# Performance work log

Hardware: AMD Instinct MI355X
Metric: run time of the kernel (lower is better)

Reference implementation:

```python
import jax, jax.numpy as jnp
import numpy as np

N_NODES = 100000
N_EDGES = 1600000
IN_DIM = 64
OUT_DIM = 64
HIDDEN = 64  # fixed in edge_weight_mlp
POS_DIM = 3


def setup_inputs() -> dict:
    key = jax.random.key(0)
    ks = jax.random.split(key, 10)
    x = jax.random.normal(ks[0], (N_NODES, IN_DIM), dtype=jnp.float32)
    edge_index = jax.random.randint(ks[1], (2, N_EDGES), 0, N_NODES, dtype=jnp.int64)
    pos = jax.random.normal(ks[2], (N_NODES, POS_DIM), dtype=jnp.float32)
    # edge_weight_mlp params: Linear(2*IN_DIM+1 -> 64), Linear(64 -> 1)
    s1 = 1.0 / np.sqrt(2 * IN_DIM + 1)
    w1 = jax.random.uniform(ks[3], (2 * IN_DIM + 1, HIDDEN), jnp.float32, -s1, s1)
    b1 = jax.random.uniform(ks[4], (HIDDEN,), jnp.float32, -s1, s1)
    s2 = 1.0 / np.sqrt(HIDDEN)
    w2 = jax.random.uniform(ks[5], (HIDDEN, 1), jnp.float32, -s2, s2)
    b2 = jax.random.uniform(ks[6], (1,), jnp.float32, -s2, s2)
    # transform: Linear(IN_DIM -> OUT_DIM)
    st = 1.0 / np.sqrt(IN_DIM)
    wt = jax.random.uniform(ks[7], (IN_DIM, OUT_DIM), jnp.float32, -st, st)
    bt = jax.random.uniform(ks[8], (OUT_DIM,), jnp.float32, -st, st)
    return {"x": x, "edge_index": edge_index, "pos": pos,
            "w1": w1, "b1": b1, "w2": w2, "b2": b2, "wt": wt, "bt": bt}


def reference(x, edge_index, pos, w1, b1, w2, b2, wt, bt):
    src, dst = edge_index[0], edge_index[1]
    # edge weights: MLP on [x_src, x_dst, |pos_dst - pos_src|]
    edge_length = jnp.linalg.norm(pos[dst] - pos[src], axis=1, keepdims=True)  # [E,1]
    edge_feat = jnp.concatenate([x[src], x[dst], edge_length], axis=1)  # [E, 2*in+1]
    h = jax.nn.relu(edge_feat @ w1 + b1)
    edge_weights = jax.nn.sigmoid(h @ w2 + b2)  # [E,1]
    # node transform, gather, weight, scatter-add
    x_t = x @ wt + bt  # [N, out]
    messages = x_t[src] * edge_weights  # [E, out]
    out = jax.ops.segment_sum(messages, dst, num_segments=x.shape[0])  # [N, out]
    return out, edge_weights
```

## Files before the change

kernel.cpp:

```cpp
#include <hip/hip_runtime.h>
#include <hip/hip_bf16.h>
#include <math.h>

#define NN 100000
#define NE 1600000
#define CAP 48
#define NB 391
#define BCAP 4608
#define EPB 4096
#define NBLKA ((NE + EPB - 1) / EPB)
#define NPREP ((NN + 63) / 64)
#define PSTR 72

typedef __attribute__((ext_vector_type(8))) short short8;
typedef __attribute__((ext_vector_type(4))) float floatx4;
typedef __attribute__((ext_vector_type(2))) float float2v;

#if __has_builtin(__builtin_elementwise_fma)
#define VFMA(a, b, c) __builtin_elementwise_fma((a), (b), (c))
#else
#define VFMA(a, b, c) ((a) * (b) + (c))
#endif

static __device__ __forceinline__ unsigned short f2bb(float f) {
    __hip_bfloat16 h = __float2bfloat16(f);
    return *(unsigned short*)&h;
}
static __device__ __forceinline__ float hi_f(unsigned u) {
    return __uint_as_float(u & 0xFFFF0000u);
}
static __device__ __forceinline__ float lo_f(unsigned u) {
    return __uint_as_float(u << 16);
}
static __device__ __forceinline__ float2v hi2(unsigned a, unsigned b) {
    float2v r; r.x = __uint_as_float(a & 0xFFFF0000u);
    r.y = __uint_as_float(b & 0xFFFF0000u); return r;
}
static __device__ __forceinline__ float2v lo2(unsigned a, unsigned b) {
    float2v r; r.x = __uint_as_float(a << 16);
    r.y = __uint_as_float(b << 16); return r;
}

__global__ __launch_bounds__(256) void fused_prep_bucket(
    const float* __restrict__ x, const float* __restrict__ w1,
    const float* __restrict__ b1, const float* __restrict__ pos,
    const int* __restrict__ ei,
    unsigned int* __restrict__ rec, unsigned short* __restrict__ hd,
    float4* __restrict__ pos4, int* __restrict__ gcursor,
    uint2* __restrict__ bucketed) {
    __shared__ __align__(16) unsigned char smem[(64 + 128) * PSTR * 2];
    int t = threadIdx.x;
    if (blockIdx.x < NPREP) {
        unsigned short* As = (unsigned short*)smem;
        unsigned short* Bs = As + 64 * PSTR;
        int nbase = blockIdx.x * 64;
        {
            int r = t & 63;
            int node = nbase + r; if (node >= NN) node = NN - 1;
            const float4* xr = (const float4*)(x + (size_t)node * 64);
#pragma unroll
            for (int i = 0; i < 4; ++i) {
                int s = (t >> 6) + 4 * i;
                float4 v = xr[s];
                ushort4 o = {f2bb(v.x), f2bb(v.y), f2bb(v.z), f2bb(v.w)};
                *(ushort4*)&As[r * PSTR + s * 4] = o;
            }
        }
        {
            int n = t & 127;
            int kh = t >> 7;
            int krow = (n < 64) ? 0 : 64;
            int col = n & 63;
#pragma unroll
            for (int i = 0; i < 32; ++i) {
                int k = kh * 32 + i;
                Bs[n * PSTR + k] = f2bb(w1[(krow + k) * 64 + col]);
            }
        }
        if (t < 64) {
            int node = nbase + t;
            if (node < NN)
                pos4[node] = make_float4(pos[node * 3 + 0], pos[node * 3 + 1],
                                         pos[node * 3 + 2], 0.f);
        }
        __syncthreads();
        int lane = t & 63, wave = t >> 6;
        int grp = lane >> 4, l15 = lane & 15;
        floatx4 acc[8] = {};
        int arow = wave * 16 + l15;
#pragma unroll
        for (int ks = 0; ks < 2; ++ks) {
            int koff = ks * 32 + grp * 8;
            short8 a = *(const short8*)&As[arow * PSTR + koff];
#pragma unroll
            for (int nt = 0; nt < 8; ++nt) {
                short8 b = *(const short8*)&Bs[(nt * 16 + l15) * PSTR + koff];
                acc[nt] = __builtin_amdgcn_mfma_f32_16x16x32_bf16(a, b, acc[nt], 0, 0, 0);
            }
        }
#pragma unroll
        for (int nt = 0; nt < 8; ++nt) {
#pragma unroll
            for (int r = 0; r < 4; ++r) {
                int nr = wave * 16 + grp * 4 + r;
                int node = nbase + nr;
                if (node >= NN) continue;
                if (nt < 4) {
                    int col = nt * 16 + l15;
                    unsigned xbits = As[nr * PSTR + col];
                    rec[(size_t)node * 64 + col] =
                        ((unsigned)f2bb(acc[nt][r]) << 16) | xbits;
                } else {
                    int col = (nt - 4) * 16 + l15;
                    hd[(size_t)node * 64 + col] = f2bb(acc[nt][r] + b1[col]);
                }
            }
        }
    } else {
        int* cnt = (int*)smem;
        int* base_s = cnt + NB;
        for (int i = t; i < NB; i += 256) cnt[i] = 0;
        __syncthreads();
        int e0 = (blockIdx.x - NPREP) * EPB;
        unsigned int tags[16];
        int srcs[16], dsts[16];
#pragma unroll
        for (int i = 0; i < 16; ++i) {
            int e = e0 + i * 256 + t;
            tags[i] = 0xFFFFFFFFu;
            if (e < NE) {
                srcs[i] = ei[e];
                dsts[i] = ei[NE + e];
                int b = dsts[i] >> 8;
                int slot = atomicAdd(&cnt[b], 1);
                tags[i] = ((unsigned)b << 12) | (unsigned)slot;
            }
        }
        __syncthreads();
        for (int b = t; b < NB; b += 256)
            base_s[b] = atomicAdd(&gcursor[b], cnt[b]);
        __syncthreads();
#pragma unroll
        for (int i = 0; i < 16; ++i) {
            if (tags[i] != 0xFFFFFFFFu) {
                int e = e0 + i * 256 + t;
                int b = (int)(tags[i] >> 12);
                int slot = (int)(tags[i] & 0xFFFu);
                int p = base_s[b] + slot;
                if (p < BCAP) {
                    bucketed[(size_t)b * BCAP + p] =
                        make_uint2((unsigned)srcs[i] |
                                   (((unsigned)dsts[i] & 255u) << 17),
                                   (unsigned)e);
                }
            }
        }
    }
}

__global__ __launch_bounds__(1024) void csr_kernel(
    const uint2* __restrict__ bucketed, const int* __restrict__ gcursor,
    uint2* __restrict__ pairs, int* __restrict__ deg) {
    __shared__ int cur[256];
    int t = threadIdx.x;
    if (t < 256) cur[t] = 0;
    __syncthreads();
    int b = blockIdx.x;
    int n0 = b << 8;
    int cnt = gcursor[b];
    if (cnt > BCAP) cnt = BCAP;
    for (int i = t; i < cnt; i += 1024) {
        uint2 en = bucketed[(size_t)b * BCAP + i];
        int dwb = (int)((en.x >> 17) & 255u);
        unsigned src = en.x & 0x1FFFFu;
        int slot = atomicAdd(&cur[dwb], 1);
        if (slot < CAP)
            pairs[(size_t)(n0 + dwb) * CAP + slot] = make_uint2(src, en.y);
    }
    __syncthreads();
    if (t < 256) {
        int node = n0 + t;
        if (node < NN) deg[node] = (cur[t] > CAP) ? CAP : cur[t];
    }
}

__global__ __launch_bounds__(256) void mega_kernel(
    const uint2* __restrict__ pairs, const int* __restrict__ deg,
    const unsigned int* __restrict__ rec, const unsigned short* __restrict__ hd,
    const float4* __restrict__ pos4, const float* __restrict__ w1,
    const float* __restrict__ w2, const float* __restrict__ b2,
    float* __restrict__ ew_out, unsigned short* __restrict__ aggb,
    float* __restrict__ sumw) {
    int t = threadIdx.x;
    int w = t >> 6, lane = t & 63;
    int e8 = lane >> 3, hg = lane & 7;
    int node = blockIdx.x * 4 + w;
    if (node >= NN) return;

    const float2v zero2 = {0.f, 0.f};
    float2v a01 = zero2, a23 = zero2, a45 = zero2, a67 = zero2;
    float sw = 0.f;
    int d = deg[node];
    uint4 hz = ((const uint4*)(hd + (size_t)node * 64))[hg];
    float2v zb01 = {lo_f(hz.x), hi_f(hz.x)};
    float2v zb23 = {lo_f(hz.y), hi_f(hz.y)};
    float2v zb45 = {lo_f(hz.z), hi_f(hz.z)};
    float2v zb67 = {lo_f(hz.w), hi_f(hz.w)};
    const float2v* w2p = (const float2v*)(w2 + 8 * hg);
    float2v w20 = w2p[0], w21 = w2p[1], w22 = w2p[2], w23 = w2p[3];
    const float2v* wlp = (const float2v*)(w1 + 128 * 64 + 8 * hg);
    float2v wl0 = wlp[0], wl1 = wlp[1], wl2 = wlp[2], wl3 = wlp[3];
    float4 pd = pos4[node];
    float b2v = b2[0];
    const uint2* seg = pairs + (size_t)node * CAP;
    const uint4* rec4 = (const uint4*)rec;

    if (d > 0) {
        int i0 = (e8 < d) ? e8 : (d - 1);
        uint2 pr_c = seg[i0];
        uint2 pr_n = pr_c;
        if (8 < d) { int i1 = (8 + e8 < d) ? (8 + e8) : (d - 1); pr_n = seg[i1]; }
        uint4 ua_c = rec4[(size_t)pr_c.x * 16 + 2 * hg];
        uint4 ub_c = rec4[(size_t)pr_c.x * 16 + 2 * hg + 1];
        float4 ps_c = pos4[pr_c.x];

#pragma unroll 2
        for (int j = 0; j < d; j += 8) {
            int jn = j + 8;
            uint2 pr_n2 = pr_n;
            uint4 ua_n = ua_c, ub_n = ub_c;
            float4 ps_n = ps_c;
            if (jn < d) {
                ua_n = rec4[(size_t)pr_n.x * 16 + 2 * hg];
                ub_n = rec4[(size_t)pr_n.x * 16 + 2 * hg + 1];
                ps_n = pos4[pr_n.x];
                if (jn + 8 < d) {
                    int i2 = (jn + 8 + e8 < d) ? (jn + 8 + e8) : (d - 1);
                    pr_n2 = seg[i2];
                }
            }
            bool valid = (j + e8 < d);
            float dx = pd.x - ps_c.x;
            float dy = pd.y - ps_c.y;
            float dz = pd.z - ps_c.z;
            float len = __builtin_amdgcn_sqrtf(dx * dx + dy * dy + dz * dz);
            float2v l2; l2.x = len; l2.y = len;
            float2v z, r, tp;
            z = zb01 + hi2(ua_c.x, ua_c.y); z = VFMA(l2, wl0, z);
            r = __builtin_elementwise_max(z, zero2); tp = r * w20;
            z = zb23 + hi2(ua_c.z, ua_c.w); z = VFMA(l2, wl1, z);
            r = __builtin_elementwise_max(z, zero2); tp = VFMA(r, w21, tp);
            z = zb45 + hi2(ub_c.x, ub_c.y); z = VFMA(l2, wl2, z);
            r = __builtin_elementwise_max(z, zero2); tp = VFMA(r, w22, tp);
            z = zb67 + hi2(ub_c.z, ub_c.w); z = VFMA(l2, wl3, z);
            r = __builtin_elementwise_max(z, zero2); tp = VFMA(r, w23, tp);
            float tt = tp.x + tp.y;
            tt += __shfl_xor(tt, 1);
            tt += __shfl_xor(tt, 2);
            tt += __shfl_xor(tt, 4);
            float ew = __builtin_amdgcn_rcpf(1.f + __expf(-(tt + b2v)));
            if (valid) {
                if (hg == 0) ew_out[pr_c.y] = ew;
                float2v e2; e2.x = ew; e2.y = ew;
                a01 = VFMA(e2, lo2(ua_c.x, ua_c.y), a01);
                a23 = VFMA(e2, lo2(ua_c.z, ua_c.w), a23);
                a45 = VFMA(e2, lo2(ub_c.x, ub_c.y), a45);
                a67 = VFMA(e2, lo2(ub_c.z, ub_c.w), a67);
                sw += ew;
            }
            pr_c = pr_n; pr_n = pr_n2;
            ua_c = ua_n; ub_c = ub_n; ps_c = ps_n;
        }
    }
    float acc0 = a01.x, acc1 = a01.y, acc2 = a23.x, acc3 = a23.y;
    float acc4 = a45.x, acc5 = a45.y, acc6 = a67.x, acc7 = a67.y;
#pragma unroll
    for (int off = 8; off < 64; off <<= 1) {
        acc0 += __shfl_xor(acc0, off);
        acc1 += __shfl_xor(acc1, off);
        acc2 += __shfl_xor(acc2, off);
        acc3 += __shfl_xor(acc3, off);
        acc4 += __shfl_xor(acc4, off);
        acc5 += __shfl_xor(acc5, off);
        acc6 += __shfl_xor(acc6, off);
        acc7 += __shfl_xor(acc7, off);
        sw   += __shfl_xor(sw, off);
    }
    if (e8 == 0) {
        uint4 o;
        o.x = ((unsigned)f2bb(acc1) << 16) | f2bb(acc0);
        o.y = ((unsigned)f2bb(acc3) << 16) | f2bb(acc2);
        o.z = ((unsigned)f2bb(acc5) << 16) | f2bb(acc4);
        o.w = ((unsigned)f2bb(acc7) << 16) | f2bb(acc6);
        *(uint4*)(aggb + (size_t)node * 64 + hg * 8) = o;
    }
    if (lane == 0) sumw[node] = sw;
}

__global__ __launch_bounds__(256) void transform_mfma(
    const unsigned short* __restrict__ aggb, const float* __restrict__ sumw,
    const float* __restrict__ wt, const float* __restrict__ bt,
    float* __restrict__ out) {
    __shared__ unsigned short As[64 * PSTR];
    __shared__ unsigned short Bs[64 * PSTR];
    int t = threadIdx.x;
    int nbase = blockIdx.x * 64;
    {
        int r = t & 63;
        int node = nbase + r; if (node >= NN) node = NN - 1;
        const uint4* ar = (const uint4*)(aggb + (size_t)node * 64);
#pragma unroll
        for (int i = 0; i < 2; ++i) {
            int s = (t >> 6) + 4 * i;
            *(uint4*)&As[r * PSTR + s * 8] = ar[s];
        }
    }
    {
        int n = t & 63;
        int kq = t >> 6;
#pragma unroll
        for (int i = 0; i < 16; ++i) {
            int k = kq * 16 + i;
            Bs[n * PSTR + k] = f2bb(wt[k * 64 + n]);
        }
    }
    __syncthreads();
    int lane = t & 63, wave = t >> 6;
    int grp = lane >> 4, l15 = lane & 15;
    floatx4 acc[4] = {};
    int arow = wave * 16 + l15;
#pragma unroll
    for (int ks = 0; ks < 2; ++ks) {
        int koff = ks * 32 + grp * 8;
        short8 a = *(const short8*)&As[arow * PSTR + koff];
#pragma unroll
        for (int nt = 0; nt < 4; ++nt) {
            short8 b = *(const short8*)&Bs[(nt * 16 + l15) * PSTR + koff];
            acc[nt] = __builtin_amdgcn_mfma_f32_16x16x32_bf16(a, b, acc[nt], 0, 0, 0);
        }
    }
#pragma unroll
    for (int nt = 0; nt < 4; ++nt) {
        int col = nt * 16 + l15;
        float btv = bt[col];
#pragma unroll
        for (int r = 0; r < 4; ++r) {
            int node = nbase + wave * 16 + grp * 4 + r;
            if (node < NN)
                out[(size_t)node * 64 + col] = acc[nt][r] + sumw[node] * btv;
        }
    }
}

extern "C" void kernel_launch(void* const* d_in, const int* in_sizes, int n_in,
                              void* d_out, int out_size, void* d_ws, size_t ws_size,
                              hipStream_t stream) {
    const float* x   = (const float*)d_in[0];
    const int*   ei  = (const int*)d_in[1];
    const float* pos = (const float*)d_in[2];
    const float* w1  = (const float*)d_in[3];
    const float* b1  = (const float*)d_in[4];
    const float* w2  = (const float*)d_in[5];
    const float* b2  = (const float*)d_in[6];
    const float* wt  = (const float*)d_in[7];
    const float* bt  = (const float*)d_in[8];

    float* out    = (float*)d_out;
    float* ew_out = out + (size_t)NN * 64;

    unsigned int* rec = (unsigned int*)d_ws;
    unsigned short* hd = (unsigned short*)(rec + (size_t)NN * 64);
    uint2* pairs = (uint2*)(hd + (size_t)NN * 64);
    unsigned short* aggb = (unsigned short*)(pairs + (size_t)NN * CAP);
    float4* pos4 = (float4*)(aggb + (size_t)NN * 64);
    float* sumw = (float*)(pos4 + NN);
    int* gcursor = (int*)(sumw + NN);
    int* deg = gcursor + NB;

    uint2* bucketed = (uint2*)d_out;

    hipMemsetAsync(gcursor, 0, NB * sizeof(int), stream);
    fused_prep_bucket<<<NPREP + NBLKA, 256, 0, stream>>>(
        x, w1, b1, pos, ei, rec, hd, pos4, gcursor, bucketed);
    csr_kernel<<<NB, 1024, 0, stream>>>(bucketed, gcursor, pairs, deg);
    mega_kernel<<<(NN + 3) / 4, 256, 0, stream>>>(pairs, deg, rec, hd, pos4,
                                                  w1, w2, b2, ew_out, aggb, sumw);
    transform_mfma<<<(NN + 63) / 64, 256, 0, stream>>>(aggb, sumw, wt, bt, out);
}
```

Before: 246.0 us.

## Build per-node CSR directly with global atomics, dropping bucket pass and csr kernel

Replaces the two-stage bucketing (shared-memory bucket counts, global cursor, then a separate csr_kernel) with direct global atomicAdd on a per-node degree counter that writes each edge into its node's fixed-capacity slot. This removes one kernel launch and the intermediate bucketed buffer round-trip through memory. The cost is 1.6M global atomics scattered over 100K counters and scattered 8-byte writes into pairs, which may contend or give poorer write locality. Degree is now clamped to CAP in mega_kernel, and a larger memset clears the degree array.

Result: slower. 316.4 us (+28.6%).

```diff
diff --git a/kernel.cpp b/kernel.cpp
--- a/kernel.cpp
+++ b/kernel.cpp
@@ -5,8 +5,6 @@
 #define NN 100000
 #define NE 1600000
 #define CAP 48
-#define NB 391
-#define BCAP 4608
 #define EPB 4096
 #define NBLKA ((NE + EPB - 1) / EPB)
 #define NPREP ((NN + 63) / 64)
@@ -46,8 +44,8 @@
     const float* __restrict__ b1, const float* __restrict__ pos,
     const int* __restrict__ ei,
     unsigned int* __restrict__ rec, unsigned short* __restrict__ hd,
-    float4* __restrict__ pos4, int* __restrict__ gcursor,
-    uint2* __restrict__ bucketed) {
+    float4* __restrict__ pos4, int* __restrict__ deg,
+    uint2* __restrict__ pairs) {
     __shared__ __align__(16) unsigned char smem[(64 + 128) * PSTR * 2];
     int t = threadIdx.x;
     if (blockIdx.x < NPREP) {
@@ -117,70 +115,19 @@
             }
         }
     } else {
-        int* cnt = (int*)smem;
-        int* base_s = cnt + NB;
-        for (int i = t; i < NB; i += 256) cnt[i] = 0;
-        __syncthreads();
         int e0 = (blockIdx.x - NPREP) * EPB;
-        unsigned int tags[16];
-        int srcs[16], dsts[16];
-#pragma unroll
+#pragma unroll 4
         for (int i = 0; i < 16; ++i) {
             int e = e0 + i * 256 + t;
-            tags[i] = 0xFFFFFFFFu;
             if (e < NE) {
-                srcs[i] = ei[e];
-                dsts[i] = ei[NE + e];
-                int b = dsts[i] >> 8;
-                int slot = atomicAdd(&cnt[b], 1);
-                tags[i] = ((unsigned)b << 12) | (unsigned)slot;
-            }
-        }
-        __syncthreads();
-        for (int b = t; b < NB; b += 256)
-            base_s[b] = atomicAdd(&gcursor[b], cnt[b]);
-        __syncthreads();
-#pragma unroll
-        for (int i = 0; i < 16; ++i) {
-            if (tags[i] != 0xFFFFFFFFu) {
-                int e = e0 + i * 256 + t;
-                int b = (int)(tags[i] >> 12);
-                int slot = (int)(tags[i] & 0xFFFu);
-                int p = base_s[b] + slot;
-                if (p < BCAP) {
-                    bucketed[(size_t)b * BCAP + p] =
-                        make_uint2((unsigned)srcs[i] |
-                                   (((unsigned)dsts[i] & 255u) << 17),
-                                   (unsigned)e);
-                }
-            }
-        }
-    }
-}
-
-__global__ __launch_bounds__(1024) void csr_kernel(
-    const uint2* __restrict__ bucketed, const int* __restrict__ gcursor,
-    uint2* __restrict__ pairs, int* __restrict__ deg) {
-    __shared__ int cur[256];
-    int t = threadIdx.x;
-    if (t < 256) cur[t] = 0;
-    __syncthreads();
-    int b = blockIdx.x;
-    int n0 = b << 8;
-    int cnt = gcursor[b];
-    if (cnt > BCAP) cnt = BCAP;
-    for (int i = t; i < cnt; i += 1024) {
-        uint2 en = bucketed[(size_t)b * BCAP + i];
-        int dwb = (int)((en.x >> 17) & 255u);
-        unsigned src = en.x & 0x1FFFFu;
-        int slot = atomicAdd(&cur[dwb], 1);
-        if (slot < CAP)
-            pairs[(size_t)(n0 + dwb) * CAP + slot] = make_uint2(src, en.y);
-    }
-    __syncthreads();
-    if (t < 256) {
-        int node = n0 + t;
-        if (node < NN) deg[node] = (cur[t] > CAP) ? CAP : cur[t];
+                int src = ei[e];
+                int dst = ei[NE + e];
+                int slot = atomicAdd(&deg[dst], 1);
+                if (slot < CAP)
+                    pairs[(size_t)dst * CAP + slot] =
+                        make_uint2((unsigned)src, (unsigned)e);
+            }
+        }
     }
 }
 
@@ -201,6 +148,7 @@
     float2v a01 = zero2, a23 = zero2, a45 = zero2, a67 = zero2;
     float sw = 0.f;
     int d = deg[node];
+    if (d > CAP) d = CAP;
     uint4 hz = ((const uint4*)(hd + (size_t)node * 64))[hg];
     float2v zb01 = {lo_f(hz.x), hi_f(hz.x)};
     float2v zb23 = {lo_f(hz.y), hi_f(hz.y)};
@@ -374,15 +322,11 @@
     unsigned short* aggb = (unsigned short*)(pairs + (size_t)NN * CAP);
     float4* pos4 = (float4*)(aggb + (size_t)NN * 64);
     float* sumw = (float*)(pos4 + NN);
-    int* gcursor = (int*)(sumw + NN);
-    int* deg = gcursor + NB;
-
-    uint2* bucketed = (uint2*)d_out;
-
-    hipMemsetAsync(gcursor, 0, NB * sizeof(int), stream);
+    int* deg = (int*)(sumw + NN);
+
+    hipMemsetAsync(deg, 0, NN * sizeof(int), stream);
     fused_prep_bucket<<<NPREP + NBLKA, 256, 0, stream>>>(
-        x, w1, b1, pos, ei, rec, hd, pos4, gcursor, bucketed);
-    csr_kernel<<<NB, 1024, 0, stream>>>(bucketed, gcursor, pairs, deg);
+        x, w1, b1, pos, ei, rec, hd, pos4, deg, pairs);
     mega_kernel<<<(NN + 3) / 4, 256, 0, stream>>>(pairs, deg, rec, hd, pos4,
                                                   w1, w2, b2, ew_out, aggb, sumw);
     transform_mfma<<<(NN + 63) / 64, 256, 0, stream>>>(aggb, sumw, wt, bt, out);
```

## Apply node transform before aggregation and drop separate transform kernel

Applied to the files above, without the earlier changes.

The prep kernel now also multiplies x by wt with MFMA and stores bf16 x@wt in the low half of each rec word, where it previously stored bf16 x. The edge-aggregation kernel then sums already-transformed features, adds sumw*bt, and writes the fp32 output directly. This rests on linearity, since a weighted sum of x rows times wt equals the weighted sum of the transformed rows. It removes the transform_mfma launch and the write and re-read of the aggb and sumw intermediates. The cost is extra MFMA work and weight staging in the prep kernel, plus bf16 rounding now applied to x@wt instead of to x.

After: 238.8 us. 1.03x faster.

```diff
diff --git a/kernel.cpp b/kernel.cpp
--- a/kernel.cpp
+++ b/kernel.cpp
@@ -43,12 +43,12 @@
 
 __global__ __launch_bounds__(256) void fused_prep_bucket(
     const float* __restrict__ x, const float* __restrict__ w1,
-    const float* __restrict__ b1, const float* __restrict__ pos,
-    const int* __restrict__ ei,
+    const float* __restrict__ b1, const float* __restrict__ wt,
+    const float* __restrict__ pos, const int* __restrict__ ei,
     unsigned int* __restrict__ rec, unsigned short* __restrict__ hd,
     float4* __restrict__ pos4, int* __restrict__ gcursor,
     uint2* __restrict__ bucketed) {
-    __shared__ __align__(16) unsigned char smem[(64 + 128) * PSTR * 2];
+    __shared__ __align__(16) unsigned char smem[(64 + 192) * PSTR * 2];
     int t = threadIdx.x;
     if (blockIdx.x < NPREP) {
         unsigned short* As = (unsigned short*)smem;
@@ -67,14 +67,16 @@
             }
         }
         {
-            int n = t & 127;
-            int kh = t >> 7;
-            int krow = (n < 64) ? 0 : 64;
-            int col = n & 63;
-#pragma unroll
-            for (int i = 0; i < 32; ++i) {
-                int k = kh * 32 + i;
-                Bs[n * PSTR + k] = f2bb(w1[(krow + k) * 64 + col]);
+            int n = t & 63;
+            int kq = t >> 6;
+#pragma unroll
+            for (int s = 0; s < 3; ++s) {
+                const float* src = (s < 2) ? (w1 + (size_t)s * 64 * 64) : wt;
+#pragma unroll
+                for (int i = 0; i < 16; ++i) {
+                    int k = kq * 16 + i;
+                    Bs[(s * 64 + n) * PSTR + k] = f2bb(src[k * 64 + n]);
+                }
             }
         }
         if (t < 64) {
@@ -86,34 +88,29 @@
         __syncthreads();
         int lane = t & 63, wave = t >> 6;
         int grp = lane >> 4, l15 = lane & 15;
-        floatx4 acc[8] = {};
+        floatx4 acc[12] = {};
         int arow = wave * 16 + l15;
 #pragma unroll
         for (int ks = 0; ks < 2; ++ks) {
             int koff = ks * 32 + grp * 8;
             short8 a = *(const short8*)&As[arow * PSTR + koff];
 #pragma unroll
-            for (int nt = 0; nt < 8; ++nt) {
+            for (int nt = 0; nt < 12; ++nt) {
                 short8 b = *(const short8*)&Bs[(nt * 16 + l15) * PSTR + koff];
                 acc[nt] = __builtin_amdgcn_mfma_f32_16x16x32_bf16(a, b, acc[nt], 0, 0, 0);
             }
         }
 #pragma unroll
-        for (int nt = 0; nt < 8; ++nt) {
+        for (int nt = 0; nt < 4; ++nt) {
 #pragma unroll
             for (int r = 0; r < 4; ++r) {
                 int nr = wave * 16 + grp * 4 + r;
                 int node = nbase + nr;
                 if (node >= NN) continue;
-                if (nt < 4) {
-                    int col = nt * 16 + l15;
-                    unsigned xbits = As[nr * PSTR + col];
-                    rec[(size_t)node * 64 + col] =
-                        ((unsigned)f2bb(acc[nt][r]) << 16) | xbits;
-                } else {
-                    int col = (nt - 4) * 16 + l15;
-                    hd[(size_t)node * 64 + col] = f2bb(acc[nt][r] + b1[col]);
-                }
+                int col = nt * 16 + l15;
+                rec[(size_t)node * 64 + col] =
+                    ((unsigned)f2bb(acc[nt][r]) << 16) | f2bb(acc[8 + nt][r]);
+                hd[(size_t)node * 64 + col] = f2bb(acc[4 + nt][r] + b1[col]);
             }
         }
     } else {
@@ -189,8 +186,8 @@
     const unsigned int* __restrict__ rec, const unsigned short* __restrict__ hd,
     const float4* __restrict__ pos4, const float* __restrict__ w1,
     const float* __restrict__ w2, const float* __restrict__ b2,
-    float* __restrict__ ew_out, unsigned short* __restrict__ aggb,
-    float* __restrict__ sumw) {
+    const float* __restrict__ bt,
+    float* __restrict__ ew_out, float* __restrict__ out) {
     int t = threadIdx.x;
     int w = t >> 6, lane = t & 63;
     int e8 = lane >> 3, hg = lane & 7;
@@ -210,6 +207,8 @@
     float2v w20 = w2p[0], w21 = w2p[1], w22 = w2p[2], w23 = w2p[3];
     const float2v* wlp = (const float2v*)(w1 + 128 * 64 + 8 * hg);
     float2v wl0 = wlp[0], wl1 = wlp[1], wl2 = wlp[2], wl3 = wlp[3];
+    float4 bta = ((const float4*)bt)[2 * hg];
+    float4 btb = ((const float4*)bt)[2 * hg + 1];
     float4 pd = pos4[node];
     float b2v = b2[0];
     const uint2* seg = pairs + (size_t)node * CAP;
@@ -287,68 +286,13 @@
         sw   += __shfl_xor(sw, off);
     }
     if (e8 == 0) {
-        uint4 o;
-        o.x = ((unsigned)f2bb(acc1) << 16) | f2bb(acc0);
-        o.y = ((unsigned)f2bb(acc3) << 16) | f2bb(acc2);
-        o.z = ((unsigned)f2bb(acc5) << 16) | f2bb(acc4);
-        o.w = ((unsigned)f2bb(acc7) << 16) | f2bb(acc6);
-        *(uint4*)(aggb + (size_t)node * 64 + hg * 8) = o;
-    }
-    if (lane == 0) sumw[node] = sw;
-}
-
-__global__ __launch_bounds__(256) void transform_mfma(
-    const unsigned short* __restrict__ aggb, const float* __restrict__ sumw,
-    const float* __restrict__ wt, const float* __restrict__ bt,
-    float* __restrict__ out) {
-    __shared__ unsigned short As[64 * PSTR];
-    __shared__ unsigned short Bs[64 * PSTR];
-    int t = threadIdx.x;
-    int nbase = blockIdx.x * 64;
-    {
-        int r = t & 63;
-        int node = nbase + r; if (node >= NN) node = NN - 1;
-        const uint4* ar = (const uint4*)(aggb + (size_t)node * 64);
-#pragma unroll
-        for (int i = 0; i < 2; ++i) {
-            int s = (t >> 6) + 4 * i;
-            *(uint4*)&As[r * PSTR + s * 8] = ar[s];
-        }
-    }
-    {
-        int n = t & 63;
-        int kq = t >> 6;
-#pragma unroll
-        for (int i = 0; i < 16; ++i) {
-            int k = kq * 16 + i;
-            Bs[n * PSTR + k] = f2bb(wt[k * 64 + n]);
-        }
-    }
-    __syncthreads();
-    int lane = t & 63, wave = t >> 6;
-    int grp = lane >> 4, l15 = lane & 15;
-    floatx4 acc[4] = {};
-    int arow = wave * 16 + l15;
-#pragma unroll
-    for (int ks = 0; ks < 2; ++ks) {
-        int koff = ks * 32 + grp * 8;
-        short8 a = *(const short8*)&As[arow * PSTR + koff];
-#pragma unroll
-        for (int nt = 0; nt < 4; ++nt) {
-            short8 b = *(const short8*)&Bs[(nt * 16 + l15) * PSTR + koff];
-            acc[nt] = __builtin_amdgcn_mfma_f32_16x16x32_bf16(a, b, acc[nt], 0, 0, 0);
-        }
-    }
-#pragma unroll
-    for (int nt = 0; nt < 4; ++nt) {
-        int col = nt * 16 + l15;
-        float btv = bt[col];
-#pragma unroll
-        for (int r = 0; r < 4; ++r) {
-            int node = nbase + wave * 16 + grp * 4 + r;
-            if (node < NN)
-                out[(size_t)node * 64 + col] = acc[nt][r] + sumw[node] * btv;
-        }
+        float* orow = out + (size_t)node * 64 + hg * 8;
+        float4 o1 = {acc0 + sw * bta.x, acc1 + sw * bta.y,
+                     acc2 + sw * bta.z, acc3 + sw * bta.w};
+        float4 o2 = {acc4 + sw * btb.x, acc5 + sw * btb.y,
+                     acc6 + sw * btb.z, acc7 + sw * btb.w};
+        *(float4*)orow = o1;
+        *(float4*)(orow + 4) = o2;
     }
 }
 
@@ -371,19 +315,16 @@
     unsigned int* rec = (unsigned int*)d_ws;
     unsigned short* hd = (unsigned short*)(rec + (size_t)NN * 64);
     uint2* pairs = (uint2*)(hd + (size_t)NN * 64);
-    unsigned short* aggb = (unsigned short*)(pairs + (size_t)NN * CAP);
-    float4* pos4 = (float4*)(aggb + (size_t)NN * 64);
-    float* sumw = (float*)(pos4 + NN);
-    int* gcursor = (int*)(sumw + NN);
+    float4* pos4 = (float4*)(pairs + (size_t)NN * CAP);
+    int* gcursor = (int*)(pos4 + NN);
     int* deg = gcursor + NB;
 
     uint2* bucketed = (uint2*)d_out;
 
     hipMemsetAsync(gcursor, 0, NB * sizeof(int), stream);
     fused_prep_bucket<<<NPREP + NBLKA, 256, 0, stream>>>(
-        x, w1, b1, pos, ei, rec, hd, pos4, gcursor, bucketed);
+        x, w1, b1, wt, pos, ei, rec, hd, pos4, gcursor, bucketed);
     csr_kernel<<<NB, 1024, 0, stream>>>(bucketed, gcursor, pairs, deg);
     mega_kernel<<<(NN + 3) / 4, 256, 0, stream>>>(pairs, deg, rec, hd, pos4,
-                                                  w1, w2, b2, ew_out, aggb, sumw);
-    transform_mfma<<<(NN + 63) / 64, 256, 0, stream>>>(aggb, sumw, wt, bt, out);
-}
+                                                  w1, w2, b2, bt, ew_out, out);
+}
```
